# Kernel optimization log

Measured on AMD Instinct MI355X. Metric: run time of the kernel, lower is better.

The kernel has to match this reference:

```python
import jax, jax.numpy as jnp
import numpy as np

HEADS = 16

def setup_inputs() -> dict:
    key = jax.random.key(0)
    k1, k2, k3 = jax.random.split(key, 3)
    B, S, D = 2, 2048, 1024
    return {
        "query": jax.random.normal(k1, (B, S, D), dtype=jnp.float32),
        "key": jax.random.normal(k2, (B, S, D), dtype=jnp.float32),
        "value": jax.random.normal(k3, (B, S, D), dtype=jnp.float32),
    }

def reference(query, key, value):
    B, S, D = query.shape
    H = HEADS
    dh = D // H
    # split(-1) into H equal chunks == reshape to (B, S, H, dh)
    q = query.reshape(B, S, H, dh)
    k = key.reshape(B, S, H, dh)
    v = value.reshape(B, S, H, dh)
    scale = 1.0 / jnp.sqrt(jnp.asarray(dh, dtype=query.dtype))
    scores = jnp.einsum('bqhd,bkhd->bhqk', q, k) * scale  # [B,H,S,S]
    probs = jax.nn.softmax(scores, axis=-1)
    out = jnp.einsum('bhqk,bkhd->bqhd', probs, v)  # [B,S,H,dh]
    return out.reshape(B, S, D)
```

## Files before the change

kernel.cpp:

```cpp
#include <hip/hip_runtime.h>
#include <stdint.h>


#define B_ 2
#define S_ 2048
#define D_ 1024
#define H_ 16
#define DH 64
#define M_TILE 128
#define N_TILE 128
#define NITER (S_ / N_TILE)

typedef __bf16 bf16;
typedef __bf16 bf16x2 __attribute__((ext_vector_type(2)));
typedef __bf16 bf16x4 __attribute__((ext_vector_type(4)));
typedef __bf16 bf16x8 __attribute__((ext_vector_type(8)));
typedef float floatx4 __attribute__((ext_vector_type(4)));

#define KB_TOTAL (B_ * S_ * D_ * 2)
#define KROW_B (D_ * 2)
#define KB_HEAD (S_ * DH * 2)
#define VT_ROW (S_ * 2)
#define WS_NEEDED (2u * KB_TOTAL)

#define N_TILE2 64
#define NITER2 (S_ / N_TILE2)
#define KT2 8192
#define BUF2 16384
#define LSH_OFF2 (4 * BUF2)
#define SMEM_MAIN (LSH_OFF2 + 512)
#define O_STRIDE 36

__device__ __forceinline__ float fast_exp2(float x) {
#if __has_builtin(__builtin_amdgcn_exp2f)
  return __builtin_amdgcn_exp2f(x);
#else
  return exp2f(x);
#endif
}

__device__ __forceinline__ void gl_lds16(const void* g, void* l) {
  __builtin_amdgcn_global_load_lds(
      (const __attribute__((address_space(1))) unsigned int*)g,
      (__attribute__((address_space(3))) unsigned int*)l, 16, 0, 0);
}

__global__ __launch_bounds__(256)
void prep(const float* __restrict__ Kg, const float* __restrict__ Vg,
          unsigned char* __restrict__ ws) {
  const int bid = blockIdx.x;
  const int tid = threadIdx.x;
  if (bid < 512) {
    __shared__ __align__(16) bf16 VTsh[64][136];
    const int head_lin = bid & 31, ktile = bid >> 5;
    const int b = head_lin >> 4, h = head_lin & 15;
    const int kb = ktile * 128;
    const int vr0 = (tid >> 3) << 2;
    const int vf0 = (tid & 7) << 3;
    const float* Vbase = Vg + (size_t)(b * S_) * D_ + h * DH;
    float vals[4][8];
#pragma unroll
    for (int rr = 0; rr < 4; ++rr) {
      const float* vp = Vbase + (size_t)(kb + vr0 + rr) * D_ + vf0;
      float4 a = *(const float4*)vp;
      float4 c = *(const float4*)(vp + 4);
      vals[rr][0] = a.x; vals[rr][1] = a.y; vals[rr][2] = a.z; vals[rr][3] = a.w;
      vals[rr][4] = c.x; vals[rr][5] = c.y; vals[rr][6] = c.z; vals[rr][7] = c.w;
    }
    const int pbase = (vr0 & 96) + ((vr0 >> 2) & 3) * 8 + ((vr0 >> 4) & 1) * 4;
    const int psw = (((pbase >> 3) ^ (tid & 7)) << 3) | (pbase & 7);
#pragma unroll
    for (int j = 0; j < 8; ++j) {
      bf16x4 y = {(bf16)vals[0][j], (bf16)vals[1][j], (bf16)vals[2][j], (bf16)vals[3][j]};
      *(bf16x4*)(&VTsh[vf0 + j][psw]) = y;
    }
    __syncthreads();
    unsigned char* Vout = ws + KB_TOTAL + (size_t)head_lin * KB_HEAD;
#pragma unroll
    for (int j = 0; j < 4; ++j) {
      const int id    = j * 256 + tid;
      const int chunk = id & 15;
      const int f     = id >> 4;
      const int gs    = chunk ^ ((f >> 3) & 7);
      bf16x8 v = *(const bf16x8*)(&VTsh[f][gs << 3]);
      *(bf16x8*)(Vout + (size_t)f * VT_ROW + kb * 2 + chunk * 16) = v;
    }
  } else {
    const int idx = (bid - 512) * 256 + tid;
    const float* src = Kg + (size_t)idx * 8;
    float4 x0 = ((const float4*)src)[0];
    float4 x1 = ((const float4*)src)[1];
    bf16x8 y = {(bf16)x0.x, (bf16)x0.y, (bf16)x0.z, (bf16)x0.w,
                (bf16)x1.x, (bf16)x1.y, (bf16)x1.z, (bf16)x1.w};
    *(bf16x8*)(ws + (size_t)idx * 16) = y;
  }
}

__global__ __launch_bounds__(512, 4)
void attn_fwd(const float* __restrict__ Qg, const unsigned char* __restrict__ Kb,
              const unsigned char* __restrict__ VT, float* __restrict__ Og) {
  __shared__ __align__(16) unsigned char smem[SMEM_MAIN];
  float* Osh = (float*)smem;
  float* Lsh = (float*)(smem + LSH_OFF2);

  const int tid  = threadIdx.x;
  const int lane = tid & 63;
  const int wave = tid >> 6;
  const int kw   = wave & 1;
  const int qw   = wave >> 1;
  const int col  = lane & 15;
  const int quad = lane >> 4;

  const int bid      = blockIdx.x;
  const int head_lin = bid & 31;
  const int qtile    = bid >> 5;
  const int b        = head_lin >> 4;
  const int h        = head_lin & 15;

  const unsigned char* Khead = Kb + (size_t)(b * S_) * KROW_B + h * (DH * 2);
  const unsigned char* Vhead = VT + (size_t)head_lin * (DH * VT_ROW);

  const float QSCALE = 0.125f * 1.44269504088896340736f;

  bf16x8 Qf[2][2];
#pragma unroll
  for (int qt = 0; qt < 2; ++qt) {
    const float* base = Qg + (size_t)(b * S_ + qtile * M_TILE + qw * 32 + qt * 16 + col) * D_
                        + h * DH + quad * 8;
#pragma unroll
    for (int ks = 0; ks < 2; ++ks) {
      float4 x0 = *(const float4*)(base + ks * 32);
      float4 x1 = *(const float4*)(base + ks * 32 + 4);
      bf16x8 f;
      f[0] = (bf16)(x0.x * QSCALE); f[1] = (bf16)(x0.y * QSCALE);
      f[2] = (bf16)(x0.z * QSCALE); f[3] = (bf16)(x0.w * QSCALE);
      f[4] = (bf16)(x1.x * QSCALE); f[5] = (bf16)(x1.y * QSCALE);
      f[6] = (bf16)(x1.z * QSCALE); f[7] = (bf16)(x1.w * QSCALE);
      Qf[qt][ks] = f;
    }
  }

  floatx4 accO[4][2];
  float l_lane[2] = {0.f, 0.f};
#pragma unroll
  for (int ft = 0; ft < 4; ++ft)
#pragma unroll
    for (int qt = 0; qt < 2; ++qt) accO[ft][qt] = (floatx4)0.f;

  const int sub = lane >> 3;
  const int gx  = ((lane & 7) ^ sub) << 4;

  auto dma_tile2 = [&](int kbk, int bufoff) {
    const int r = (wave << 3) + sub;
    gl_lds16(Khead + (size_t)(kbk + r) * KROW_B + gx,
             smem + bufoff + (wave << 10));
    gl_lds16(Vhead + (size_t)r * VT_ROW + kbk * 2 + gx,
             smem + bufoff + KT2 + (wave << 10));
  };

  const int cq = col & 7;
  const int ka0_off = (kw * 32 + col) * 128 + ((quad ^ cq) << 4);
  const int ka1_off = (kw * 32 + col) * 128 + (((quad | 4) ^ cq) << 4);
  const int va0_off = KT2 + col * 128 + (((kw * 4 + quad) ^ cq) << 4);

  dma_tile2(0, 0);
  dma_tile2(N_TILE2, BUF2);

  bf16x8 Pf[2];

  for (int it = 0; it < NITER2; ++it) {
    if (it + 2 < NITER2) dma_tile2((it + 2) * N_TILE2, ((it + 2) & 3) * BUF2);
    const int bc = (it & 3) * BUF2;
    const int bp = ((it - 1) & 3) * BUF2;

    __builtin_amdgcn_sched_barrier(0);
    if (it + 2 < NITER2)       asm volatile("s_waitcnt vmcnt(4)" ::: "memory");
    else if (it + 2 == NITER2) asm volatile("s_waitcnt vmcnt(2)" ::: "memory");
    else                       asm volatile("s_waitcnt vmcnt(0)" ::: "memory");
    __builtin_amdgcn_s_barrier();
    asm volatile("" ::: "memory");
    __builtin_amdgcn_sched_barrier(0);

    floatx4 accS[2][2];
    __builtin_amdgcn_s_setprio(1);
#pragma unroll
    for (int kt = 0; kt < 2; ++kt) {
      bf16x8 Ka0 = *(const bf16x8*)(smem + bc + ka0_off + kt * 2048);
      bf16x8 Ka1 = *(const bf16x8*)(smem + bc + ka1_off + kt * 2048);
#pragma unroll
      for (int qt = 0; qt < 2; ++qt) {
        floatx4 a = (floatx4)0.f;
        a = __builtin_amdgcn_mfma_f32_16x16x32_bf16(Ka0, Qf[qt][0], a, 0, 0, 0);
        a = __builtin_amdgcn_mfma_f32_16x16x32_bf16(Ka1, Qf[qt][1], a, 0, 0, 0);
        accS[kt][qt] = a;
      }
    }

    if (it > 0) {
#pragma unroll
      for (int ft = 0; ft < 4; ++ft) {
        bf16x8 Va = *(const bf16x8*)(smem + bp + va0_off + ft * 2048);
#pragma unroll
        for (int qt = 0; qt < 2; ++qt)
          accO[ft][qt] = __builtin_amdgcn_mfma_f32_16x16x32_bf16(Va, Pf[qt], accO[ft][qt], 0, 0, 0);
      }
    }
    __builtin_amdgcn_s_setprio(0);

#pragma unroll
    for (int qt = 0; qt < 2; ++qt) {
      float rs = 0.f;
#pragma unroll
      for (int kt = 0; kt < 2; ++kt)
#pragma unroll
        for (int r = 0; r < 4; ++r) {
          float p = fast_exp2(accS[kt][qt][r]);
          accS[kt][qt][r] = p;
          rs += p;
        }
      l_lane[qt] += rs;
    }
#pragma unroll
    for (int qt = 0; qt < 2; ++qt) {
      floatx4 p0 = accS[0][qt], p1 = accS[1][qt];
      bf16x8 f = {(bf16)p0[0], (bf16)p0[1], (bf16)p0[2], (bf16)p0[3],
                  (bf16)p1[0], (bf16)p1[1], (bf16)p1[2], (bf16)p1[3]};
      Pf[qt] = f;
    }

    __builtin_amdgcn_sched_barrier(0);
    asm volatile("" ::: "memory");
    __builtin_amdgcn_s_barrier();
  }

  {
    const int bp = ((NITER2 - 1) & 3) * BUF2;
    __builtin_amdgcn_s_setprio(1);
#pragma unroll
    for (int ft = 0; ft < 4; ++ft) {
      bf16x8 Va = *(const bf16x8*)(smem + bp + va0_off + ft * 2048);
#pragma unroll
      for (int qt = 0; qt < 2; ++qt)
        accO[ft][qt] = __builtin_amdgcn_mfma_f32_16x16x32_bf16(Va, Pf[qt], accO[ft][qt], 0, 0, 0);
    }
    __builtin_amdgcn_s_setprio(0);
  }
  __syncthreads();

  float l_red[2];
#pragma unroll
  for (int qt = 0; qt < 2; ++qt) {
    float s = l_lane[qt];
    s += __shfl_xor(s, 16);
    s += __shfl_xor(s, 32);
    l_red[qt] = s;
  }

  if (kw == 1) {
    float* r = Osh + (qw * 64 + lane) * O_STRIDE;
#pragma unroll
    for (int qt = 0; qt < 2; ++qt)
#pragma unroll
      for (int ft = 0; ft < 4; ++ft)
        *(floatx4*)(r + (qt * 4 + ft) * 4) = accO[ft][qt];
    if (quad == 0) {
#pragma unroll
      for (int qt = 0; qt < 2; ++qt)
        Lsh[qw * 32 + qt * 16 + col] = l_red[qt];
    }
  }
  __syncthreads();

  if (kw == 0) {
    const float* r = Osh + (qw * 64 + lane) * O_STRIDE;
    float rl[2];
#pragma unroll
    for (int qt = 0; qt < 2; ++qt)
      rl[qt] = 1.0f / (l_red[qt] + Lsh[qw * 32 + qt * 16 + col]);
#pragma unroll
    for (int qt = 0; qt < 2; ++qt) {
      const int q = qtile * M_TILE + qw * 32 + qt * 16 + col;
      float* dst = Og + (size_t)(b * S_ + q) * D_ + h * DH + quad * 4;
#pragma unroll
      for (int ft = 0; ft < 4; ++ft) {
        floatx4 o = (accO[ft][qt] + *(const floatx4*)(r + (qt * 4 + ft) * 4)) * rl[qt];
        *(floatx4*)(dst + ft * 16) = o;
      }
    }
  }
}

#define FB_K_STRIDE 68
#define FB_V_STRIDE 132
#define FB_K_BYTES (128 * FB_K_STRIDE * 2)
#define FB_V_BYTES (64 * FB_V_STRIDE * 2)
#define FB_SMEM ((256 * O_STRIDE * 4 + 2048) > (FB_K_BYTES + FB_V_BYTES) ? (256 * O_STRIDE * 4 + 2048) : (FB_K_BYTES + FB_V_BYTES))

__device__ __forceinline__ bf16x8 cat8(bf16x4 a, bf16x4 b) {
  return __builtin_shufflevector(a, b, 0, 1, 2, 3, 4, 5, 6, 7);
}

__global__ __launch_bounds__(512, 4)
void attn_fwd_fb(const float* __restrict__ Qg, const float* __restrict__ Kg,
                 const float* __restrict__ Vg, float* __restrict__ Og) {
  __shared__ __align__(16) unsigned char smem[FB_SMEM];
  bf16*  Ksh = (bf16*)smem;
  bf16*  Vsh = (bf16*)(smem + FB_K_BYTES);
  float* Osh = (float*)smem;
  float* Lsh = (float*)(smem + 256 * O_STRIDE * 4);

  const int tid  = threadIdx.x;
  const int lane = tid & 63;
  const int wave = tid >> 6;
  const int kw   = wave & 1;
  const int qw   = wave >> 1;
  const int col  = lane & 15;
  const int quad = lane >> 4;
  const int bid      = blockIdx.x;
  const int head_lin = bid & 31;
  const int qtile    = bid >> 5;
  const int b        = head_lin >> 4;
  const int h        = head_lin & 15;
  const float QSCALE = 0.125f * 1.44269504088896340736f;

  bf16x8 Qf[2][2];
#pragma unroll
  for (int qt = 0; qt < 2; ++qt) {
    const float* base = Qg + (size_t)(b * S_ + qtile * 128 + qw * 32 + qt * 16 + col) * D_
                        + h * DH + quad * 8;
#pragma unroll
    for (int ks = 0; ks < 2; ++ks) {
      float4 x0 = *(const float4*)(base + ks * 32);
      float4 x1 = *(const float4*)(base + ks * 32 + 4);
      bf16x8 f;
      f[0] = (bf16)(x0.x * QSCALE); f[1] = (bf16)(x0.y * QSCALE);
      f[2] = (bf16)(x0.z * QSCALE); f[3] = (bf16)(x0.w * QSCALE);
      f[4] = (bf16)(x1.x * QSCALE); f[5] = (bf16)(x1.y * QSCALE);
      f[6] = (bf16)(x1.z * QSCALE); f[7] = (bf16)(x1.w * QSCALE);
      Qf[qt][ks] = f;
    }
  }

  floatx4 accO[4][2];
  float l_lane[2] = {0.f, 0.f};
#pragma unroll
  for (int ft = 0; ft < 4; ++ft)
#pragma unroll
    for (int qt = 0; qt < 2; ++qt) accO[ft][qt] = (floatx4)0.f;

  const float* Kbase = Kg + (size_t)(b * S_) * D_ + h * DH;
  const float* Vbase = Vg + (size_t)(b * S_) * D_ + h * DH;
  const int krow0 = tid >> 4;
  const int kf4   = tid & 15;
  const int vk0   = (tid >> 3) * 2;
  const int vf0   = (tid & 7) * 8;

  for (int it = 0; it < NITER; ++it) {
    const int kb = it * 128;
    float4 kx[4];
#pragma unroll
    for (int i = 0; i < 4; ++i)
      kx[i] = *(const float4*)(Kbase + (size_t)(kb + krow0 + 32 * i) * D_ + kf4 * 4);
    float4 va0 = *(const float4*)(Vbase + (size_t)(kb + vk0) * D_ + vf0);
    float4 va1 = *(const float4*)(Vbase + (size_t)(kb + vk0) * D_ + vf0 + 4);
    float4 vb0 = *(const float4*)(Vbase + (size_t)(kb + vk0 + 1) * D_ + vf0);
    float4 vb1 = *(const float4*)(Vbase + (size_t)(kb + vk0 + 1) * D_ + vf0 + 4);
#pragma unroll
    for (int i = 0; i < 4; ++i) {
      bf16x4 y = {(bf16)kx[i].x, (bf16)kx[i].y, (bf16)kx[i].z, (bf16)kx[i].w};
      *(bf16x4*)(Ksh + (krow0 + 32 * i) * FB_K_STRIDE + kf4 * 4) = y;
    }
    {
      float a[8] = {va0.x, va0.y, va0.z, va0.w, va1.x, va1.y, va1.z, va1.w};
      float c[8] = {vb0.x, vb0.y, vb0.z, vb0.w, vb1.x, vb1.y, vb1.z, vb1.w};
#pragma unroll
      for (int j = 0; j < 8; ++j) {
        bf16x2 y = {(bf16)a[j], (bf16)c[j]};
        *(bf16x2*)(Vsh + (vf0 + j) * FB_V_STRIDE + vk0) = y;
      }
    }
    __syncthreads();

    floatx4 accS[4][2];
#pragma unroll
    for (int kt = 0; kt < 4; ++kt) {
      const bf16* kp = Ksh + (kw * 64 + kt * 16 + col) * FB_K_STRIDE + quad * 8;
      bf16x8 Ka0 = cat8(*(const bf16x4*)kp, *(const bf16x4*)(kp + 4));
      bf16x8 Ka1 = cat8(*(const bf16x4*)(kp + 32), *(const bf16x4*)(kp + 36));
#pragma unroll
      for (int qt = 0; qt < 2; ++qt) {
        floatx4 a = (floatx4)0.f;
        a = __builtin_amdgcn_mfma_f32_16x16x32_bf16(Ka0, Qf[qt][0], a, 0, 0, 0);
        a = __builtin_amdgcn_mfma_f32_16x16x32_bf16(Ka1, Qf[qt][1], a, 0, 0, 0);
        accS[kt][qt] = a;
      }
    }
#pragma unroll
    for (int qt = 0; qt < 2; ++qt) {
      float rs = 0.f;
#pragma unroll
      for (int kt = 0; kt < 4; ++kt)
#pragma unroll
        for (int r = 0; r < 4; ++r) {
          float p = fast_exp2(accS[kt][qt][r]);
          accS[kt][qt][r] = p;
          rs += p;
        }
      l_lane[qt] += rs;
    }
#pragma unroll
    for (int c = 0; c < 2; ++c) {
      bf16x8 Pf[2];
#pragma unroll
      for (int qt = 0; qt < 2; ++qt) {
        floatx4 p0 = accS[2 * c][qt], p1 = accS[2 * c + 1][qt];
        bf16x8 f = {(bf16)p0[0], (bf16)p0[1], (bf16)p0[2], (bf16)p0[3],
                    (bf16)p1[0], (bf16)p1[1], (bf16)p1[2], (bf16)p1[3]};
        Pf[qt] = f;
      }
#pragma unroll
      for (int ft = 0; ft < 4; ++ft) {
        const bf16* vp = Vsh + (ft * 16 + col) * FB_V_STRIDE + kw * 64 + 32 * c + quad * 4;
        bf16x8 Va = cat8(*(const bf16x4*)vp, *(const bf16x4*)(vp + 16));
#pragma unroll
        for (int qt = 0; qt < 2; ++qt)
          accO[ft][qt] = __builtin_amdgcn_mfma_f32_16x16x32_bf16(Va, Pf[qt], accO[ft][qt], 0, 0, 0);
      }
    }
    __syncthreads();
  }

  float l_red[2];
#pragma unroll
  for (int qt = 0; qt < 2; ++qt) {
    float s = l_lane[qt];
    s += __shfl_xor(s, 16);
    s += __shfl_xor(s, 32);
    l_red[qt] = s;
  }
  if (kw == 1) {
    float* r = Osh + (qw * 64 + lane) * O_STRIDE;
#pragma unroll
    for (int qt = 0; qt < 2; ++qt)
#pragma unroll
      for (int ft = 0; ft < 4; ++ft)
        *(floatx4*)(r + (qt * 4 + ft) * 4) = accO[ft][qt];
    if (quad == 0) {
#pragma unroll
      for (int qt = 0; qt < 2; ++qt)
        Lsh[qw * 32 + qt * 16 + col] = l_red[qt];
    }
  }
  __syncthreads();
  if (kw == 0) {
    const float* r = Osh + (qw * 64 + lane) * O_STRIDE;
    float rl[2];
#pragma unroll
    for (int qt = 0; qt < 2; ++qt)
      rl[qt] = 1.0f / (l_red[qt] + Lsh[qw * 32 + qt * 16 + col]);
#pragma unroll
    for (int qt = 0; qt < 2; ++qt) {
      const int q = qtile * 128 + qw * 32 + qt * 16 + col;
      float* dst = Og + (size_t)(b * S_ + q) * D_ + h * DH + quad * 4;
#pragma unroll
      for (int ft = 0; ft < 4; ++ft) {
        floatx4 o = (accO[ft][qt] + *(const floatx4*)(r + (qt * 4 + ft) * 4)) * rl[qt];
        *(floatx4*)(dst + ft * 16) = o;
      }
    }
  }
}

extern "C" void kernel_launch(void* const* d_in, const int* in_sizes, int n_in,
                              void* d_out, int out_size, void* d_ws, size_t ws_size,
                              hipStream_t stream) {
  const float* Q = (const float*)d_in[0];
  const float* K = (const float*)d_in[1];
  const float* V = (const float*)d_in[2];
  float* O = (float*)d_out;
  if (ws_size >= WS_NEEDED && d_ws != nullptr) {
    unsigned char* ws = (unsigned char*)d_ws;
    hipLaunchKernelGGL(prep, dim3(2560), dim3(256), 0, stream, K, V, ws);
    hipLaunchKernelGGL(attn_fwd, dim3(B_ * H_ * (S_ / M_TILE)), dim3(512), 0, stream,
                       Q, ws, ws + KB_TOTAL, O);
  } else {
    hipLaunchKernelGGL(attn_fwd_fb, dim3(512), dim3(512), 0, stream, Q, K, V, O);
  }
}
```

Measured before the change: 127.4 us.

## Fuse K/V bf16 conversion and V transpose into attention kernel, drop prep pass

Removes the separate prep kernel that converted K and V to bf16 in a workspace, with V transposed. The attention kernel now loads fp32 K/V straight from global memory into registers, converts them, and writes swizzled bf16 tiles into LDS, prefetching one tile ahead. This replaces the async global-to-LDS DMA with a 2-deep lookahead and per-iteration __syncthreads. It saves a launch and a round trip of K/V through the workspace. In exchange it doubles global read bytes per block, since each of the 16 q-tiles reads fp32 instead of bf16. It also makes strided scalar V loads and loses the deeper async pipelining.

```diff
diff --git a/kernel.cpp b/kernel.cpp
--- a/kernel.cpp
+++ b/kernel.cpp
@@ -8,20 +8,6 @@
 #define H_ 16
 #define DH 64
 #define M_TILE 128
-#define N_TILE 128
-#define NITER (S_ / N_TILE)
-
-typedef __bf16 bf16;
-typedef __bf16 bf16x2 __attribute__((ext_vector_type(2)));
-typedef __bf16 bf16x4 __attribute__((ext_vector_type(4)));
-typedef __bf16 bf16x8 __attribute__((ext_vector_type(8)));
-typedef float floatx4 __attribute__((ext_vector_type(4)));
-
-#define KB_TOTAL (B_ * S_ * D_ * 2)
-#define KROW_B (D_ * 2)
-#define KB_HEAD (S_ * DH * 2)
-#define VT_ROW (S_ * 2)
-#define WS_NEEDED (2u * KB_TOTAL)
 
 #define N_TILE2 64
 #define NITER2 (S_ / N_TILE2)
@@ -31,6 +17,10 @@
 #define SMEM_MAIN (LSH_OFF2 + 512)
 #define O_STRIDE 36
 
+typedef __bf16 bf16;
+typedef __bf16 bf16x8 __attribute__((ext_vector_type(8)));
+typedef float floatx4 __attribute__((ext_vector_type(4)));
+
 __device__ __forceinline__ float fast_exp2(float x) {
 #if __has_builtin(__builtin_amdgcn_exp2f)
   return __builtin_amdgcn_exp2f(x);
@@ -39,66 +29,9 @@
 #endif
 }
 
-__device__ __forceinline__ void gl_lds16(const void* g, void* l) {
-  __builtin_amdgcn_global_load_lds(
-      (const __attribute__((address_space(1))) unsigned int*)g,
-      (__attribute__((address_space(3))) unsigned int*)l, 16, 0, 0);
-}
-
-__global__ __launch_bounds__(256)
-void prep(const float* __restrict__ Kg, const float* __restrict__ Vg,
-          unsigned char* __restrict__ ws) {
-  const int bid = blockIdx.x;
-  const int tid = threadIdx.x;
-  if (bid < 512) {
-    __shared__ __align__(16) bf16 VTsh[64][136];
-    const int head_lin = bid & 31, ktile = bid >> 5;
-    const int b = head_lin >> 4, h = head_lin & 15;
-    const int kb = ktile * 128;
-    const int vr0 = (tid >> 3) << 2;
-    const int vf0 = (tid & 7) << 3;
-    const float* Vbase = Vg + (size_t)(b * S_) * D_ + h * DH;
-    float vals[4][8];
-#pragma unroll
-    for (int rr = 0; rr < 4; ++rr) {
-      const float* vp = Vbase + (size_t)(kb + vr0 + rr) * D_ + vf0;
-      float4 a = *(const float4*)vp;
-      float4 c = *(const float4*)(vp + 4);
-      vals[rr][0] = a.x; vals[rr][1] = a.y; vals[rr][2] = a.z; vals[rr][3] = a.w;
-      vals[rr][4] = c.x; vals[rr][5] = c.y; vals[rr][6] = c.z; vals[rr][7] = c.w;
-    }
-    const int pbase = (vr0 & 96) + ((vr0 >> 2) & 3) * 8 + ((vr0 >> 4) & 1) * 4;
-    const int psw = (((pbase >> 3) ^ (tid & 7)) << 3) | (pbase & 7);
-#pragma unroll
-    for (int j = 0; j < 8; ++j) {
-      bf16x4 y = {(bf16)vals[0][j], (bf16)vals[1][j], (bf16)vals[2][j], (bf16)vals[3][j]};
-      *(bf16x4*)(&VTsh[vf0 + j][psw]) = y;
-    }
-    __syncthreads();
-    unsigned char* Vout = ws + KB_TOTAL + (size_t)head_lin * KB_HEAD;
-#pragma unroll
-    for (int j = 0; j < 4; ++j) {
-      const int id    = j * 256 + tid;
-      const int chunk = id & 15;
-      const int f     = id >> 4;
-      const int gs    = chunk ^ ((f >> 3) & 7);
-      bf16x8 v = *(const bf16x8*)(&VTsh[f][gs << 3]);
-      *(bf16x8*)(Vout + (size_t)f * VT_ROW + kb * 2 + chunk * 16) = v;
-    }
-  } else {
-    const int idx = (bid - 512) * 256 + tid;
-    const float* src = Kg + (size_t)idx * 8;
-    float4 x0 = ((const float4*)src)[0];
-    float4 x1 = ((const float4*)src)[1];
-    bf16x8 y = {(bf16)x0.x, (bf16)x0.y, (bf16)x0.z, (bf16)x0.w,
-                (bf16)x1.x, (bf16)x1.y, (bf16)x1.z, (bf16)x1.w};
-    *(bf16x8*)(ws + (size_t)idx * 16) = y;
-  }
-}
-
 __global__ __launch_bounds__(512, 4)
-void attn_fwd(const float* __restrict__ Qg, const unsigned char* __restrict__ Kb,
-              const unsigned char* __restrict__ VT, float* __restrict__ Og) {
+void attn_fwd(const float* __restrict__ Qg, const float* __restrict__ Kg,
+              const float* __restrict__ Vg, float* __restrict__ Og) {
   __shared__ __align__(16) unsigned char smem[SMEM_MAIN];
   float* Osh = (float*)smem;
   float* Lsh = (float*)(smem + LSH_OFF2);
@@ -116,9 +49,6 @@
   const int qtile    = bid >> 5;
   const int b        = head_lin >> 4;
   const int h        = head_lin & 15;
-
-  const unsigned char* Khead = Kb + (size_t)(b * S_) * KROW_B + h * (DH * 2);
-  const unsigned char* Vhead = VT + (size_t)head_lin * (DH * VT_ROW);
 
   const float QSCALE = 0.125f * 1.44269504088896340736f;
 
@@ -148,37 +78,52 @@
     for (int qt = 0; qt < 2; ++qt) accO[ft][qt] = (floatx4)0.f;
 
   const int sub = lane >> 3;
-  const int gx  = ((lane & 7) ^ sub) << 4;
-
-  auto dma_tile2 = [&](int kbk, int bufoff) {
-    const int r = (wave << 3) + sub;
-    gl_lds16(Khead + (size_t)(kbk + r) * KROW_B + gx,
-             smem + bufoff + (wave << 10));
-    gl_lds16(Vhead + (size_t)r * VT_ROW + kbk * 2 + gx,
-             smem + bufoff + KT2 + (wave << 10));
-  };
+  const int lo3 = lane & 7;
+  const int krow = (wave << 3) + sub;
+  const float* Ksrc = Kg + (size_t)(b * S_ + krow) * D_ + h * DH + lo3 * 8;
+  const int g4 = ((wave >> 2) << 5) + ((wave & 3) << 2);
+  const float* Vsrc = Vg + (size_t)(b * S_) * D_ + h * DH + lane;
+
+  const int kwr_off = krow * 128 + ((lo3 ^ sub) << 4);
+  const int vwr_off = KT2 + lane * 128 + ((wave ^ (lane & 7)) << 4);
 
   const int cq = col & 7;
   const int ka0_off = (kw * 32 + col) * 128 + ((quad ^ cq) << 4);
   const int ka1_off = (kw * 32 + col) * 128 + (((quad | 4) ^ cq) << 4);
   const int va0_off = KT2 + col * 128 + (((kw * 4 + quad) ^ cq) << 4);
 
-  dma_tile2(0, 0);
-  dma_tile2(N_TILE2, BUF2);
+  {
+    float4 k0 = *(const float4*)(Ksrc);
+    float4 k1 = *(const float4*)(Ksrc + 4);
+    float vv[8];
+#pragma unroll
+    for (int p = 0; p < 8; ++p)
+      vv[p] = Vsrc[(size_t)(g4 + (p & 3) + ((p >> 2) << 4)) * D_];
+    bf16x8 kb = {(bf16)k0.x, (bf16)k0.y, (bf16)k0.z, (bf16)k0.w,
+                 (bf16)k1.x, (bf16)k1.y, (bf16)k1.z, (bf16)k1.w};
+    *(bf16x8*)(smem + kwr_off) = kb;
+    bf16x8 vb = {(bf16)vv[0], (bf16)vv[1], (bf16)vv[2], (bf16)vv[3],
+                 (bf16)vv[4], (bf16)vv[5], (bf16)vv[6], (bf16)vv[7]};
+    *(bf16x8*)(smem + vwr_off) = vb;
+  }
+  __syncthreads();
 
   bf16x8 Pf[2];
 
   for (int it = 0; it < NITER2; ++it) {
-    if (it + 2 < NITER2) dma_tile2((it + 2) * N_TILE2, ((it + 2) & 3) * BUF2);
     const int bc = (it & 3) * BUF2;
     const int bp = ((it - 1) & 3) * BUF2;
-
-    __builtin_amdgcn_sched_barrier(0);
-    if (it + 2 < NITER2)       asm volatile("s_waitcnt vmcnt(4)" ::: "memory");
-    else if (it + 2 == NITER2) asm volatile("s_waitcnt vmcnt(2)" ::: "memory");
-    else                       asm volatile("s_waitcnt vmcnt(0)" ::: "memory");
-    __builtin_amdgcn_s_barrier();
-    asm volatile("" ::: "memory");
+    const int bn = ((it + 1) & 3) * BUF2;
+
+    float4 k0, k1; float vv[8];
+    if (it + 1 < NITER2) {
+      const size_t koff = (size_t)(it + 1) * N_TILE2 * D_;
+      k0 = *(const float4*)(Ksrc + koff);
+      k1 = *(const float4*)(Ksrc + koff + 4);
+#pragma unroll
+      for (int p = 0; p < 8; ++p)
+        vv[p] = Vsrc[koff + (size_t)(g4 + (p & 3) + ((p >> 2) << 4)) * D_];
+    }
     __builtin_amdgcn_sched_barrier(0);
 
     floatx4 accS[2][2];
@@ -227,10 +172,17 @@
                   (bf16)p1[0], (bf16)p1[1], (bf16)p1[2], (bf16)p1[3]};
       Pf[qt] = f;
     }
-
     __builtin_amdgcn_sched_barrier(0);
-    asm volatile("" ::: "memory");
-    __builtin_amdgcn_s_barrier();
+
+    if (it + 1 < NITER2) {
+      bf16x8 kb = {(bf16)k0.x, (bf16)k0.y, (bf16)k0.z, (bf16)k0.w,
+                   (bf16)k1.x, (bf16)k1.y, (bf16)k1.z, (bf16)k1.w};
+      *(bf16x8*)(smem + bn + kwr_off) = kb;
+      bf16x8 vb = {(bf16)vv[0], (bf16)vv[1], (bf16)vv[2], (bf16)vv[3],
+                   (bf16)vv[4], (bf16)vv[5], (bf16)vv[6], (bf16)vv[7]};
+      *(bf16x8*)(smem + bn + vwr_off) = vb;
+    }
+    __syncthreads();
   }
 
   {
@@ -280,187 +232,6 @@
 #pragma unroll
     for (int qt = 0; qt < 2; ++qt) {
       const int q = qtile * M_TILE + qw * 32 + qt * 16 + col;
-      float* dst = Og + (size_t)(b * S_ + q) * D_ + h * DH + quad * 4;
-#pragma unroll
-      for (int ft = 0; ft < 4; ++ft) {
-        floatx4 o = (accO[ft][qt] + *(const floatx4*)(r + (qt * 4 + ft) * 4)) * rl[qt];
-        *(floatx4*)(dst + ft * 16) = o;
-      }
-    }
-  }
-}
-
-#define FB_K_STRIDE 68
-#define FB_V_STRIDE 132
-#define FB_K_BYTES (128 * FB_K_STRIDE * 2)
-#define FB_V_BYTES (64 * FB_V_STRIDE * 2)
-#define FB_SMEM ((256 * O_STRIDE * 4 + 2048) > (FB_K_BYTES + FB_V_BYTES) ? (256 * O_STRIDE * 4 + 2048) : (FB_K_BYTES + FB_V_BYTES))
-
-__device__ __forceinline__ bf16x8 cat8(bf16x4 a, bf16x4 b) {
-  return __builtin_shufflevector(a, b, 0, 1, 2, 3, 4, 5, 6, 7);
-}
-
-__global__ __launch_bounds__(512, 4)
-void attn_fwd_fb(const float* __restrict__ Qg, const float* __restrict__ Kg,
-                 const float* __restrict__ Vg, float* __restrict__ Og) {
-  __shared__ __align__(16) unsigned char smem[FB_SMEM];
-  bf16*  Ksh = (bf16*)smem;
-  bf16*  Vsh = (bf16*)(smem + FB_K_BYTES);
-  float* Osh = (float*)smem;
-  float* Lsh = (float*)(smem + 256 * O_STRIDE * 4);
-
-  const int tid  = threadIdx.x;
-  const int lane = tid & 63;
-  const int wave = tid >> 6;
-  const int kw   = wave & 1;
-  const int qw   = wave >> 1;
-  const int col  = lane & 15;
-  const int quad = lane >> 4;
-  const int bid      = blockIdx.x;
-  const int head_lin = bid & 31;
-  const int qtile    = bid >> 5;
-  const int b        = head_lin >> 4;
-  const int h        = head_lin & 15;
-  const float QSCALE = 0.125f * 1.44269504088896340736f;
-
-  bf16x8 Qf[2][2];
-#pragma unroll
-  for (int qt = 0; qt < 2; ++qt) {
-    const float* base = Qg + (size_t)(b * S_ + qtile * 128 + qw * 32 + qt * 16 + col) * D_
-                        + h * DH + quad * 8;
-#pragma unroll
-    for (int ks = 0; ks < 2; ++ks) {
-      float4 x0 = *(const float4*)(base + ks * 32);
-      float4 x1 = *(const float4*)(base + ks * 32 + 4);
-      bf16x8 f;
-      f[0] = (bf16)(x0.x * QSCALE); f[1] = (bf16)(x0.y * QSCALE);
-      f[2] = (bf16)(x0.z * QSCALE); f[3] = (bf16)(x0.w * QSCALE);
-      f[4] = (bf16)(x1.x * QSCALE); f[5] = (bf16)(x1.y * QSCALE);
-      f[6] = (bf16)(x1.z * QSCALE); f[7] = (bf16)(x1.w * QSCALE);
-      Qf[qt][ks] = f;
-    }
-  }
-
-  floatx4 accO[4][2];
-  float l_lane[2] = {0.f, 0.f};
-#pragma unroll
-  for (int ft = 0; ft < 4; ++ft)
-#pragma unroll
-    for (int qt = 0; qt < 2; ++qt) accO[ft][qt] = (floatx4)0.f;
-
-  const float* Kbase = Kg + (size_t)(b * S_) * D_ + h * DH;
-  const float* Vbase = Vg + (size_t)(b * S_) * D_ + h * DH;
-  const int krow0 = tid >> 4;
-  const int kf4   = tid & 15;
-  const int vk0   = (tid >> 3) * 2;
-  const int vf0   = (tid & 7) * 8;
-
-  for (int it = 0; it < NITER; ++it) {
-    const int kb = it * 128;
-    float4 kx[4];
-#pragma unroll
-    for (int i = 0; i < 4; ++i)
-      kx[i] = *(const float4*)(Kbase + (size_t)(kb + krow0 + 32 * i) * D_ + kf4 * 4);
-    float4 va0 = *(const float4*)(Vbase + (size_t)(kb + vk0) * D_ + vf0);
-    float4 va1 = *(const float4*)(Vbase + (size_t)(kb + vk0) * D_ + vf0 + 4);
-    float4 vb0 = *(const float4*)(Vbase + (size_t)(kb + vk0 + 1) * D_ + vf0);
-    float4 vb1 = *(const float4*)(Vbase + (size_t)(kb + vk0 + 1) * D_ + vf0 + 4);
-#pragma unroll
-    for (int i = 0; i < 4; ++i) {
-      bf16x4 y = {(bf16)kx[i].x, (bf16)kx[i].y, (bf16)kx[i].z, (bf16)kx[i].w};
-      *(bf16x4*)(Ksh + (krow0 + 32 * i) * FB_K_STRIDE + kf4 * 4) = y;
-    }
-    {
-      float a[8] = {va0.x, va0.y, va0.z, va0.w, va1.x, va1.y, va1.z, va1.w};
-      float c[8] = {vb0.x, vb0.y, vb0.z, vb0.w, vb1.x, vb1.y, vb1.z, vb1.w};
-#pragma unroll
-      for (int j = 0; j < 8; ++j) {
-        bf16x2 y = {(bf16)a[j], (bf16)c[j]};
-        *(bf16x2*)(Vsh + (vf0 + j) * FB_V_STRIDE + vk0) = y;
-      }
-    }
-    __syncthreads();
-
-    floatx4 accS[4][2];
-#pragma unroll
-    for (int kt = 0; kt < 4; ++kt) {
-      const bf16* kp = Ksh + (kw * 64 + kt * 16 + col) * FB_K_STRIDE + quad * 8;
-      bf16x8 Ka0 = cat8(*(const bf16x4*)kp, *(const bf16x4*)(kp + 4));
-      bf16x8 Ka1 = cat8(*(const bf16x4*)(kp + 32), *(const bf16x4*)(kp + 36));
-#pragma unroll
-      for (int qt = 0; qt < 2; ++qt) {
-        floatx4 a = (floatx4)0.f;
-        a = __builtin_amdgcn_mfma_f32_16x16x32_bf16(Ka0, Qf[qt][0], a, 0, 0, 0);
-        a = __builtin_amdgcn_mfma_f32_16x16x32_bf16(Ka1, Qf[qt][1], a, 0, 0, 0);
-        accS[kt][qt] = a;
-      }
-    }
-#pragma unroll
-    for (int qt = 0; qt < 2; ++qt) {
-      float rs = 0.f;
-#pragma unroll
-      for (int kt = 0; kt < 4; ++kt)
-#pragma unroll
-        for (int r = 0; r < 4; ++r) {
-          float p = fast_exp2(accS[kt][qt][r]);
-          accS[kt][qt][r] = p;
-          rs += p;
-        }
-      l_lane[qt] += rs;
-    }
-#pragma unroll
-    for (int c = 0; c < 2; ++c) {
-      bf16x8 Pf[2];
-#pragma unroll
-      for (int qt = 0; qt < 2; ++qt) {
-        floatx4 p0 = accS[2 * c][qt], p1 = accS[2 * c + 1][qt];
-        bf16x8 f = {(bf16)p0[0], (bf16)p0[1], (bf16)p0[2], (bf16)p0[3],
-                    (bf16)p1[0], (bf16)p1[1], (bf16)p1[2], (bf16)p1[3]};
-        Pf[qt] = f;
-      }
-#pragma unroll
-      for (int ft = 0; ft < 4; ++ft) {
-        const bf16* vp = Vsh + (ft * 16 + col) * FB_V_STRIDE + kw * 64 + 32 * c + quad * 4;
-        bf16x8 Va = cat8(*(const bf16x4*)vp, *(const bf16x4*)(vp + 16));
-#pragma unroll
-        for (int qt = 0; qt < 2; ++qt)
-          accO[ft][qt] = __builtin_amdgcn_mfma_f32_16x16x32_bf16(Va, Pf[qt], accO[ft][qt], 0, 0, 0);
-      }
-    }
-    __syncthreads();
-  }
-
-  float l_red[2];
-#pragma unroll
-  for (int qt = 0; qt < 2; ++qt) {
-    float s = l_lane[qt];
-    s += __shfl_xor(s, 16);
-    s += __shfl_xor(s, 32);
-    l_red[qt] = s;
-  }
-  if (kw == 1) {
-    float* r = Osh + (qw * 64 + lane) * O_STRIDE;
-#pragma unroll
-    for (int qt = 0; qt < 2; ++qt)
-#pragma unroll
-      for (int ft = 0; ft < 4; ++ft)
-        *(floatx4*)(r + (qt * 4 + ft) * 4) = accO[ft][qt];
-    if (quad == 0) {
-#pragma unroll
-      for (int qt = 0; qt < 2; ++qt)
-        Lsh[qw * 32 + qt * 16 + col] = l_red[qt];
-    }
-  }
-  __syncthreads();
-  if (kw == 0) {
-    const float* r = Osh + (qw * 64 + lane) * O_STRIDE;
-    float rl[2];
-#pragma unroll
-    for (int qt = 0; qt < 2; ++qt)
-      rl[qt] = 1.0f / (l_red[qt] + Lsh[qw * 32 + qt * 16 + col]);
-#pragma unroll
-    for (int qt = 0; qt < 2; ++qt) {
-      const int q = qtile * 128 + qw * 32 + qt * 16 + col;
       float* dst = Og + (size_t)(b * S_ + q) * D_ + h * DH + quad * 4;
 #pragma unroll
       for (int ft = 0; ft < 4; ++ft) {
@@ -478,12 +249,7 @@
   const float* K = (const float*)d_in[1];
   const float* V = (const float*)d_in[2];
   float* O = (float*)d_out;
-  if (ws_size >= WS_NEEDED && d_ws != nullptr) {
-    unsigned char* ws = (unsigned char*)d_ws;
-    hipLaunchKernelGGL(prep, dim3(2560), dim3(256), 0, stream, K, V, ws);
-    hipLaunchKernelGGL(attn_fwd, dim3(B_ * H_ * (S_ / M_TILE)), dim3(512), 0, stream,
-                       Q, ws, ws + KB_TOTAL, O);
-  } else {
-    hipLaunchKernelGGL(attn_fwd_fb, dim3(512), dim3(512), 0, stream, Q, K, V, O);
-  }
+  (void)d_ws; (void)ws_size;
+  hipLaunchKernelGGL(attn_fwd, dim3(B_ * H_ * (S_ / M_TILE)), dim3(512), 0, stream,
+                     Q, K, V, O);
 }
```

New measurement: 126.7 us, median of 3. Within noise of the previous version (-0.6%).
